# Optimization experiments

Hardware: AMD Instinct MI355X
Metric: run time of the kernel (lower is better)

The kernel has to match this reference:

```python
import jax, jax.numpy as jnp
import numpy as np

DEPTH, E, H, S, V, B = 6, 1024, 16, 2048, 32000, 2
HD = E // H
EPS = 1e-5


def _layernorm(x, w, b):
    mu = jnp.mean(x, axis=-1, keepdims=True)
    var = jnp.mean(jnp.square(x - mu), axis=-1, keepdims=True)
    return (x - mu) * jax.lax.rsqrt(var + EPS) * w + b


def setup_inputs() -> dict:
    key = jax.random.key(0)
    ks = jax.random.split(key, 8)
    std = 0.02
    return {
        "idx": jax.random.randint(ks[0], (B, S), 0, V),
        "tok_emb": jax.random.normal(ks[1], (V, E), jnp.float32) * std,
        "pos_emb": jax.random.normal(ks[2], (S, E), jnp.float32) * std,
        "qkv_w": jax.random.normal(ks[3], (DEPTH, 3 * E, E), jnp.float32) * std,
        "qkv_b": jnp.zeros((DEPTH, 3 * E), jnp.float32),
        "ln1_w": jnp.ones((DEPTH, E), jnp.float32),
        "ln1_b": jnp.zeros((DEPTH, E), jnp.float32),
        "ln2_w": jnp.ones((DEPTH, E), jnp.float32),
        "ln2_b": jnp.zeros((DEPTH, E), jnp.float32),
        "ff1_w": jax.random.normal(ks[4], (DEPTH, 4 * E, E), jnp.float32) * std,
        "ff1_b": jnp.zeros((DEPTH, 4 * E), jnp.float32),
        "ff2_w": jax.random.normal(ks[5], (DEPTH, E, 4 * E), jnp.float32) * std,
        "ff2_b": jnp.zeros((DEPTH, E), jnp.float32),
        "fin_w": jnp.ones((E,), jnp.float32),
        "fin_b": jnp.zeros((E,), jnp.float32),
        "proj_w": jax.random.normal(ks[6], (V, E), jnp.float32) * std,
    }


def _block(x, qkv_w, qkv_b, ln1_w, ln1_b, ln2_w, ln2_b, ff1_w, ff1_b, ff2_w, ff2_b):
    bs, seq, _ = x.shape
    # --- causal MSA (dropout in eval mode -> identity) ---
    xn = _layernorm(x, ln1_w, ln1_b)
    qkv = xn @ qkv_w.T + qkv_b                      # [B,S,3E]
    qkv = qkv.reshape(bs, seq, 3, H, HD)
    q, k, v = (jnp.moveaxis(qkv[:, :, i], 1, 2) for i in range(3))  # [B,H,S,HD]
    scores = jnp.einsum("bhqd,bhkd->bhqk", q, k) / jnp.sqrt(jnp.float32(HD))
    causal = jnp.triu(jnp.ones((seq, seq), bool), k=1)
    scores = jnp.where(causal[None, None], -jnp.inf, scores)
    probs = jax.nn.softmax(scores, axis=-1)
    attn = jnp.einsum("bhqk,bhkd->bqhd", probs, v).reshape(bs, seq, E)
    x = x + attn
    # --- feedforward ---
    xn = _layernorm(x, ln2_w, ln2_b)
    h = jax.nn.gelu(xn @ ff1_w.T + ff1_b, approximate=False)
    x = x + (h @ ff2_w.T + ff2_b)
    return x


def reference(idx, tok_emb, pos_emb, qkv_w, qkv_b, ln1_w, ln1_b, ln2_w, ln2_b,
              ff1_w, ff1_b, ff2_w, ff2_b, fin_w, fin_b, proj_w):
    bs, seq = idx.shape
    x = tok_emb[idx] + pos_emb[jnp.arange(seq)][None]  # [B,S,E]
    for l in range(DEPTH):
        x = _block(x, qkv_w[l], qkv_b[l], ln1_w[l], ln1_b[l], ln2_w[l], ln2_b[l],
                   ff1_w[l], ff1_b[l], ff2_w[l], ff2_b[l])
    x = _layernorm(x, fin_w, fin_b)
    logits = x @ proj_w.T  # [B,S,V], final_proj has no bias
    return logits
```

## Files before the change

kernel.cpp:

```cpp
#include <hip/hip_runtime.h>
#include <hip/hip_bf16.h>

#define DEPTH 6
#define E 1024
#define H 16
#define S 2048
#define V 32000
#define BB 2
#define HD 64
#define NTOK (BB * S)

typedef __attribute__((ext_vector_type(8))) short bf16x8;
typedef __attribute__((ext_vector_type(4))) float f32x4;
typedef unsigned short us;

__device__ inline us f2bf(float f) {
    union { float f; unsigned u; } v; v.f = f;
    unsigned r = v.u + 0x7fff + ((v.u >> 16) & 1);
    return (us)(r >> 16);
}
__device__ inline float bf2f(us b) {
    union { unsigned u; float f; } v; v.u = ((unsigned)b) << 16;
    return v.f;
}

__device__ __forceinline__ void gld16(const us* g, us* l) {
    __builtin_amdgcn_global_load_lds(
        (const __attribute__((address_space(1))) unsigned int*)g,
        (__attribute__((address_space(3))) unsigned int*)l, 16, 0, 0);
}

__global__ __launch_bounds__(256) void cast_kernel(const float* __restrict__ in,
                                                   us* __restrict__ out, int n8) {
    int i = blockIdx.x * 256 + threadIdx.x;
    if (i >= n8) return;
    const float4* p = (const float4*)in + 2 * (size_t)i;
    float4 a = p[0], b = p[1];
    uint4 o;
    o.x = f2bf(a.x) | ((unsigned)f2bf(a.y) << 16);
    o.y = f2bf(a.z) | ((unsigned)f2bf(a.w) << 16);
    o.z = f2bf(b.x) | ((unsigned)f2bf(b.y) << 16);
    o.w = f2bf(b.z) | ((unsigned)f2bf(b.w) << 16);
    ((uint4*)out)[i] = o;
}

__global__ void embed_kernel(const int* __restrict__ idx, const float* __restrict__ tok,
                             const float* __restrict__ pos, float* __restrict__ x) {
    int t = blockIdx.x;
    int s = t & (S - 1);
    int tokid = idx[t];
    int c = threadIdx.x * 4;
    float4 a = *(const float4*)&tok[(size_t)tokid * E + c];
    float4 p = *(const float4*)&pos[(size_t)s * E + c];
    float4 o; o.x = a.x + p.x; o.y = a.y + p.y; o.z = a.z + p.z; o.w = a.w + p.w;
    *(float4*)&x[(size_t)t * E + c] = o;
}

__global__ __launch_bounds__(256) void ln_kernel(const float* __restrict__ x,
                                                 const float* __restrict__ w,
                                                 const float* __restrict__ b,
                                                 us* __restrict__ out) {
    int row = blockIdx.x;
    int tid = threadIdx.x;
    int c = tid * 4;
    float4 v = *(const float4*)&x[(size_t)row * E + c];
    float s  = v.x + v.y + v.z + v.w;
    float sq = v.x * v.x + v.y * v.y + v.z * v.z + v.w * v.w;
    __shared__ float red[8];
    for (int o = 32; o > 0; o >>= 1) { s += __shfl_xor(s, o); sq += __shfl_xor(sq, o); }
    int wave = tid >> 6, lane = tid & 63;
    if (lane == 0) { red[wave] = s; red[4 + wave] = sq; }
    __syncthreads();
    if (tid == 0) {
        red[0] = red[0] + red[1] + red[2] + red[3];
        red[4] = red[4] + red[5] + red[6] + red[7];
    }
    __syncthreads();
    float mean = red[0] * (1.0f / E);
    float var  = red[4] * (1.0f / E) - mean * mean;
    float rstd = rsqrtf(var + 1e-5f);
    float4 wv = *(const float4*)&w[c];
    float4 bv = *(const float4*)&b[c];
    unsigned a0 = f2bf((v.x - mean) * rstd * wv.x + bv.x);
    unsigned a1 = f2bf((v.y - mean) * rstd * wv.y + bv.y);
    unsigned a2 = f2bf((v.z - mean) * rstd * wv.z + bv.z);
    unsigned a3 = f2bf((v.w - mean) * rstd * wv.w + bv.w);
    uint2 o; o.x = a0 | (a1 << 16); o.y = a2 | (a3 << 16);
    *(uint2*)&out[(size_t)row * E + c] = o;
}

#define GPH(dd, fb, STAGE, ISVM, IS12)                                              \
  {                                                                                 \
    bf16x8 afr0[2], afr1[2];                                                        \
    if ((fb) == 0) {                                                                \
      _Pragma("unroll")                                                             \
      for (int n = 0; n < 4; n++)                                                   \
        _Pragma("unroll")                                                           \
        for (int ks = 0; ks < 2; ks++)                                              \
          bfr[n][ks] = *(const bf16x8*)&lds[32768 + (dd) * 16384 +                  \
              (brow + n * 16) * 64 + ((ks * 4 + g4) ^ xg) * 8];                     \
    }                                                                               \
    _Pragma("unroll")                                                               \
    for (int ks = 0; ks < 2; ks++) {                                                \
      afr0[ks] = *(const bf16x8*)&lds[(dd) * 16384 + ((fb) >> 1) * 4096 +           \
          arow0 * 64 + ((ks * 4 + g4) ^ xg) * 8];                                   \
      afr1[ks] = *(const bf16x8*)&lds[(dd) * 16384 + ((fb) >> 1) * 4096 +           \
          arow1 * 64 + ((ks * 4 + g4) ^ xg) * 8];                                   \
    }                                                                               \
    STAGE;                                                                          \
    __builtin_amdgcn_sched_barrier(0);                                              \
    if (IS12) asm volatile("s_waitcnt lgkmcnt(8)" ::: "memory");                    \
    __builtin_amdgcn_s_barrier();                                                   \
    asm volatile("s_waitcnt lgkmcnt(0)" ::: "memory");                              \
    __builtin_amdgcn_sched_barrier(0);                                              \
    __builtin_amdgcn_s_setprio(1);                                                  \
    _Pragma("unroll")                                                               \
    for (int n = 0; n < 4; n++)                                                     \
      _Pragma("unroll")                                                             \
      for (int ks = 0; ks < 2; ks++) {                                              \
        acc[(fb)][n]     = __builtin_amdgcn_mfma_f32_16x16x32_bf16(afr0[ks], bfr[n][ks], acc[(fb)][n], 0, 0, 0);     \
        acc[(fb) + 1][n] = __builtin_amdgcn_mfma_f32_16x16x32_bf16(afr1[ks], bfr[n][ks], acc[(fb) + 1][n], 0, 0, 0); \
      }                                                                             \
    __builtin_amdgcn_s_setprio(0);                                                  \
    __builtin_amdgcn_sched_barrier(0);                                              \
    if (ISVM) asm volatile("s_waitcnt vmcnt(6)" ::: "memory");                      \
    __builtin_amdgcn_s_barrier();                                                   \
  }

template <int OUT_BF16, int ACT_GELU, int HAS_BIAS>
__global__ __launch_bounds__(512, 2) void gemm256(const us* __restrict__ A, int lda,
                                                  const us* __restrict__ Bw, int ldb,
                                                  const float* __restrict__ bias,
                                                  void* __restrict__ outp,
                                                  int M, int N, int K, int ldo) {
    __shared__ us lds[65536];
    int tid = threadIdx.x;
    int nwg = gridDim.x;
    int wgid = blockIdx.x;
    int chunk = nwg >> 3;
    int sw = (wgid & 7) * chunk + (wgid >> 3);
    int MB = M >> 8;
    int bm = (sw % MB) * 256;
    int bn = (sw / MB) * 256;
    int w = tid >> 6, lane = tid & 63;
    int wr = w >> 2, wc = w & 3;
    int l15 = lane & 15, g4 = lane >> 4;
    int xg = l15 & 7;
    int arow0 = (wr ? 32 : 0) + l15;
    int arow1 = arow0 + 16;
    int brow = wc * 64 + l15;
    int NT = K >> 6;

    f32x4 acc[8][4] = {};
    bf16x8 bfr[4][2];

    auto stA = [&](int u, int dd, int h) {
        int uu = (u < NT) ? u : NT - 1;
        #pragma unroll
        for (int i = 0; i < 2; i++) {
            int k = tid + i * 512;
            int q = 2 * h + (k >> 9);
            int r = (k >> 3) & 63;
            int tr = q * 32 + (r & 31) + ((r >> 5) << 7);
            int gp = (k & 7) ^ (r & 7);
            gld16(A + (size_t)(bm + tr) * lda + uu * 64 + gp * 8,
                  &lds[dd * 16384 + h * 8192 + k * 8]);
        }
    };
    auto stB = [&](int u, int dd, int h) {
        int uu = (u < NT) ? u : NT - 1;
        #pragma unroll
        for (int i = 0; i < 2; i++) {
            int k = tid + i * 512;
            int row = h * 128 + (k >> 3);
            int gp = (k & 7) ^ ((k >> 3) & 7);
            gld16(Bw + (size_t)(bn + row) * ldb + uu * 64 + gp * 8,
                  &lds[32768 + dd * 16384 + h * 8192 + k * 8]);
        }
    };

    stB(0, 0, 0); stB(0, 0, 1); stA(0, 0, 0); stA(0, 0, 1);
    stB(1, 1, 0); stB(1, 1, 1); stA(1, 1, 0);
    __builtin_amdgcn_sched_barrier(0);
    asm volatile("s_waitcnt vmcnt(6)" ::: "memory");
    __builtin_amdgcn_s_barrier();

    #pragma unroll 1
    for (int t = 0; t < NT; t += 2) {
        GPH(0, 0, stA(t + 1, 1, 1), 0, 1)
        GPH(0, 2, stB(t + 2, 0, 0), 0, 0)
        GPH(0, 4, stB(t + 2, 0, 1), 0, 0)
        GPH(0, 6, stA(t + 2, 0, 0), 1, 0)
        GPH(1, 0, stA(t + 2, 0, 1), 0, 1)
        GPH(1, 2, stB(t + 3, 1, 0), 0, 0)
        GPH(1, 4, stB(t + 3, 1, 1), 0, 0)
        GPH(1, 6, stA(t + 3, 1, 0), 1, 0)
    }

    float* outf = (float*)outp;
    us* outb = (us*)outp;
    #pragma unroll
    for (int mf = 0; mf < 8; mf++)
        #pragma unroll
        for (int n = 0; n < 4; n++)
            #pragma unroll
            for (int j = 0; j < 4; j++) {
                int r = bm + wr * 128 + mf * 16 + g4 * 4 + j;
                int c = bn + wc * 64 + n * 16 + l15;
                float v = acc[mf][n][j];
                if (HAS_BIAS) v += bias[c];
                if (ACT_GELU) v = 0.5f * v * (1.0f + erff(v * 0.70710678118f));
                if (OUT_BF16) outb[(size_t)r * ldo + c] = f2bf(v);
                else outf[(size_t)r * ldo + c] = v;
            }
}

template <int SPLITK>
__global__ __launch_bounds__(256) void gemm_bf16(const us* __restrict__ A, int lda,
                                                 const us* __restrict__ Bw, int ldb,
                                                 void* __restrict__ outp,
                                                 int M, int N, int K, int ldo) {
    __shared__ us As[2 * 128 * 32];
    __shared__ us Bs[2 * 128 * 32];
    int tid = threadIdx.x;
    int nwg = gridDim.x;
    int chunk = nwg >> 3;
    int wgid = blockIdx.x;
    int sw = (wgid & 7) * chunk + (wgid >> 3);

    int bm, bn;
    us* outb = (us*)outp;
    {
        int kz = sw >> 8;
        int rem = sw & 255;
        bm = (rem & 31) * 128;
        bn = (rem >> 5) * 128;
        A  += (size_t)kz * K;
        Bw += (size_t)kz * K;
        outb += (size_t)kz * M * ldo;
    }

    int wave = tid >> 6, lane = tid & 63;
    int wr = wave >> 1, wc = wave & 1;
    int l15 = lane & 15, g4 = lane >> 4;
    f32x4 acc[4][4] = {};

    for (int k0 = 0; k0 < K; k0 += 64) {
        #pragma unroll
        for (int p4 = 0; p4 < 4; p4++) {
            int p = p4 * 256 + tid;
            int ks = p >> 9, q = p & 511;
            int row = q >> 2, c8 = (q & 3) * 8;
            gld16(&A[(size_t)(bm + row) * lda + k0 + ks * 32 + c8], &As[p * 8]);
            gld16(&Bw[(size_t)(bn + row) * ldb + k0 + ks * 32 + c8], &Bs[p * 8]);
        }
        __syncthreads();
        bf16x8 a[4][2], bfr[4][2];
        #pragma unroll
        for (int m = 0; m < 4; m++)
            #pragma unroll
            for (int ks = 0; ks < 2; ks++)
                a[m][ks] = *(const bf16x8*)&As[ks * 4096 + (wr * 64 + m * 16 + l15) * 32 + g4 * 8];
        #pragma unroll
        for (int n = 0; n < 4; n++)
            #pragma unroll
            for (int ks = 0; ks < 2; ks++)
                bfr[n][ks] = *(const bf16x8*)&Bs[ks * 4096 + (wc * 64 + n * 16 + l15) * 32 + g4 * 8];
        #pragma unroll
        for (int m = 0; m < 4; m++)
            #pragma unroll
            for (int n = 0; n < 4; n++)
                #pragma unroll
                for (int ks = 0; ks < 2; ks++)
                    acc[m][n] = __builtin_amdgcn_mfma_f32_16x16x32_bf16(a[m][ks], bfr[n][ks], acc[m][n], 0, 0, 0);
        __syncthreads();
    }

    #pragma unroll
    for (int m = 0; m < 4; m++)
        #pragma unroll
        for (int n = 0; n < 4; n++)
            #pragma unroll
            for (int j = 0; j < 4; j++) {
                int r = bm + wr * 64 + m * 16 + g4 * 4 + j;
                int c = bn + wc * 64 + n * 16 + l15;
                outb[(size_t)r * ldo + c] = f2bf(acc[m][n][j]);
            }
}

__global__ __launch_bounds__(256) void combine_ff2(const us* __restrict__ p0,
                                                   const us* __restrict__ p1,
                                                   const float* __restrict__ bias,
                                                   float* __restrict__ x) {
    int g = blockIdx.x * 256 + threadIdx.x;
    size_t base = (size_t)g * 8;
    int col = (int)(base & (E - 1));
    uint4 a = *(const uint4*)&p0[base];
    uint4 b = *(const uint4*)&p1[base];
    const us* pa = (const us*)&a;
    const us* pb = (const us*)&b;
    float4 x0 = *(const float4*)&x[base];
    float4 x1 = *(const float4*)&x[base + 4];
    float4 w0 = *(const float4*)&bias[col];
    float4 w1 = *(const float4*)&bias[col + 4];
    x0.x += bf2f(pa[0]) + bf2f(pb[0]) + w0.x;
    x0.y += bf2f(pa[1]) + bf2f(pb[1]) + w0.y;
    x0.z += bf2f(pa[2]) + bf2f(pb[2]) + w0.z;
    x0.w += bf2f(pa[3]) + bf2f(pb[3]) + w0.w;
    x1.x += bf2f(pa[4]) + bf2f(pb[4]) + w1.x;
    x1.y += bf2f(pa[5]) + bf2f(pb[5]) + w1.y;
    x1.z += bf2f(pa[6]) + bf2f(pb[6]) + w1.z;
    x1.w += bf2f(pa[7]) + bf2f(pb[7]) + w1.w;
    *(float4*)&x[base] = x0;
    *(float4*)&x[base + 4] = x1;
}

__global__ __launch_bounds__(256) void transpose_v(const us* __restrict__ qkv,
                                                   us* __restrict__ vT) {
    int kt = blockIdx.x, h = blockIdx.y, b = blockIdx.z;
    int tid = threadIdx.x;
    __shared__ us T[64][72];
    const size_t base = (size_t)b * S * 3072 + 2048 + h * 64;
    int k0 = kt * 64;
    #pragma unroll
    for (int it = 0; it < 2; it++) {
        int p = tid + it * 256;
        int key = p & 63, c8 = (p >> 6) * 8;
        uint4 v = *(const uint4*)&qkv[base + (size_t)(k0 + key) * 3072 + c8];
        us* pv = (us*)&v;
        #pragma unroll
        for (int e = 0; e < 8; e++) T[c8 + e][key] = pv[e];
    }
    __syncthreads();
    const size_t obase = ((size_t)(b * H + h) * 64) * S + k0;
    #pragma unroll
    for (int it = 0; it < 2; it++) {
        int o = tid + it * 256;
        int d = o >> 3, cc = (o & 7) * 8;
        uint4 v = *(const uint4*)&T[d][cc];
        *(uint4*)&vT[obase + (size_t)d * S + cc] = v;
    }
}

__global__ __launch_bounds__(512, 4) void attn_kernel(const us* __restrict__ qkv,
                                                      const us* __restrict__ vT,
                                                      float* __restrict__ x) {
    int qt = blockIdx.x, h = blockIdx.y, b = blockIdx.z;
    int tid = threadIdx.x;
    int w = tid >> 6, lane = tid & 63;
    int l15 = lane & 15, g4 = lane >> 4;
    int s0 = qt * 128;
    int qrow_base = s0 + w * 16;
    const size_t qbase = (size_t)b * S * 3072;
    const size_t vtbase = ((size_t)(b * H + h) * 64) * S;

    __shared__ us K_lds[2][64 * 64];
    __shared__ us VT_lds[2][64 * 64];
    __shared__ us P_lds[8][16 * 72];

    bf16x8 q[2];
    #pragma unroll
    for (int dc = 0; dc < 2; dc++)
        q[dc] = *(const bf16x8*)&qkv[qbase + (size_t)(qrow_base + l15) * 3072 + h * 64 + dc * 32 + 8 * g4];

    f32x4 O[4] = {};
    float m_run[4], l_run[4];
    #pragma unroll
    for (int j = 0; j < 4; j++) { m_run[j] = -INFINITY; l_run[j] = 0.0f; }

    int lastt = 2 * qt + 1;
    {
        int p = tid, row = p >> 3, cc = p & 7;
        int scc = cc ^ (row & 7);
        gld16(&qkv[qbase + (size_t)(0 + row) * 3072 + 1024 + h * 64 + scc * 8], &K_lds[0][p * 8]);
        gld16(&vT[vtbase + (size_t)row * S + 0 + scc * 8], &VT_lds[0][p * 8]);
    }
    __syncthreads();

    for (int t = 0; t <= lastt; t++) {
        int bb = t & 1;
        if (t < lastt) {
            int p = tid, row = p >> 3, cc = p & 7;
            int scc = cc ^ (row & 7);
            gld16(&qkv[qbase + (size_t)((t + 1) * 64 + row) * 3072 + 1024 + h * 64 + scc * 8], &K_lds[bb ^ 1][p * 8]);
            gld16(&vT[vtbase + (size_t)row * S + (t + 1) * 64 + scc * 8], &VT_lds[bb ^ 1][p * 8]);
        }
        int k0 = t * 64;
        if (k0 <= qrow_base + 15) {
            f32x4 sf[4];
            __builtin_amdgcn_s_setprio(1);
            #pragma unroll
            for (int c = 0; c < 4; c++) {
                f32x4 z = {};
                int row = c * 16 + l15;
                #pragma unroll
                for (int dc = 0; dc < 2; dc++) {
                    int ch = (dc * 4 + g4) ^ (row & 7);
                    bf16x8 kb = *(const bf16x8*)&K_lds[bb][row * 64 + ch * 8];
                    z = __builtin_amdgcn_mfma_f32_16x16x32_bf16(q[dc], kb, z, 0, 0, 0);
                }
                sf[c] = z;
            }
            __builtin_amdgcn_s_setprio(0);
            bool needmask = (k0 + 63 > qrow_base);
            float pr[4][4], alpha[4];
            #pragma unroll
            for (int j = 0; j < 4; j++) {
                int qrow = qrow_base + g4 * 4 + j;
                float v0 = sf[0][j] * 0.125f, v1 = sf[1][j] * 0.125f;
                float v2 = sf[2][j] * 0.125f, v3 = sf[3][j] * 0.125f;
                if (needmask) {
                    if (k0 +      l15 > qrow) v0 = -INFINITY;
                    if (k0 + 16 + l15 > qrow) v1 = -INFINITY;
                    if (k0 + 32 + l15 > qrow) v2 = -INFINITY;
                    if (k0 + 48 + l15 > qrow) v3 = -INFINITY;
                }
                float tm = fmaxf(fmaxf(v0, v1), fmaxf(v2, v3));
                tm = fmaxf(tm, __shfl_xor(tm, 1, 16));
                tm = fmaxf(tm, __shfl_xor(tm, 2, 16));
                tm = fmaxf(tm, __shfl_xor(tm, 4, 16));
                tm = fmaxf(tm, __shfl_xor(tm, 8, 16));
                float mnew = fmaxf(m_run[j], tm);
                float p0 = __expf(v0 - mnew), p1 = __expf(v1 - mnew);
                float p2 = __expf(v2 - mnew), p3 = __expf(v3 - mnew);
                float ts = (p0 + p1) + (p2 + p3);
                ts += __shfl_xor(ts, 1, 16);
                ts += __shfl_xor(ts, 2, 16);
                ts += __shfl_xor(ts, 4, 16);
                ts += __shfl_xor(ts, 8, 16);
                alpha[j] = __expf(m_run[j] - mnew);
                l_run[j] = l_run[j] * alpha[j] + ts;
                m_run[j] = mnew;
                pr[0][j] = p0; pr[1][j] = p1; pr[2][j] = p2; pr[3][j] = p3;
            }
            #pragma unroll
            for (int f = 0; f < 4; f++)
                #pragma unroll
                for (int j = 0; j < 4; j++) O[f][j] *= alpha[j];
            us* Pw = &P_lds[w][0];
            #pragma unroll
            for (int c = 0; c < 4; c++)
                #pragma unroll
                for (int j = 0; j < 4; j++)
                    Pw[(g4 * 4 + j) * 72 + c * 16 + l15] = f2bf(pr[c][j]);
            __builtin_amdgcn_s_setprio(1);
            #pragma unroll
            for (int kc = 0; kc < 2; kc++) {
                bf16x8 pa = *(const bf16x8*)&Pw[l15 * 72 + kc * 32 + g4 * 8];
                #pragma unroll
                for (int dt = 0; dt < 4; dt++) {
                    int row = dt * 16 + l15;
                    int ch = (kc * 4 + g4) ^ (row & 7);
                    bf16x8 vb = *(const bf16x8*)&VT_lds[bb][row * 64 + ch * 8];
                    O[dt] = __builtin_amdgcn_mfma_f32_16x16x32_bf16(pa, vb, O[dt], 0, 0, 0);
                }
            }
            __builtin_amdgcn_s_setprio(0);
        }
        __syncthreads();
    }
    #pragma unroll
    for (int dt = 0; dt < 4; dt++)
        #pragma unroll
        for (int j = 0; j < 4; j++) {
            size_t o = ((size_t)b * S + qrow_base + g4 * 4 + j) * E + h * 64 + dt * 16 + l15;
            x[o] += O[dt][j] / l_run[j];
        }
}

extern "C" void kernel_launch(void* const* d_in, const int* in_sizes, int n_in,
                              void* d_out, int out_size, void* d_ws, size_t ws_size,
                              hipStream_t stream) {
    const int*   idx    = (const int*)d_in[0];
    const float* tok    = (const float*)d_in[1];
    const float* pos    = (const float*)d_in[2];
    const float* qkv_w  = (const float*)d_in[3];
    const float* qkv_b  = (const float*)d_in[4];
    const float* ln1_w  = (const float*)d_in[5];
    const float* ln1_b  = (const float*)d_in[6];
    const float* ln2_w  = (const float*)d_in[7];
    const float* ln2_b  = (const float*)d_in[8];
    const float* ff1_w  = (const float*)d_in[9];
    const float* ff1_b  = (const float*)d_in[10];
    const float* ff2_w  = (const float*)d_in[11];
    const float* ff2_b  = (const float*)d_in[12];
    const float* fin_w  = (const float*)d_in[13];
    const float* fin_b  = (const float*)d_in[14];
    const float* proj_w = (const float*)d_in[15];

    char* ws = (char*)d_ws;
    float* x    = (float*)ws;
    us*    xn   = (us*)(ws + 16777216);
    us*    qkvb = (us*)(ws + 25165824);
    us*    hbuf = (us*)(ws + 50331648);
    us*    wbuf = (us*)(ws + 83886080);
    us*    vTb  = (us*)(ws + 92274688);
    us*    pbuf = qkvb;

    embed_kernel<<<NTOK, 256, 0, stream>>>(idx, tok, pos, x);
    for (int l = 0; l < DEPTH; l++) {
        ln_kernel<<<NTOK, 256, 0, stream>>>(x, ln1_w + l * E, ln1_b + l * E, xn);
        cast_kernel<<<1536, 256, 0, stream>>>(qkv_w + (size_t)l * 3 * E * E, wbuf, 3 * E * E / 8);
        gemm256<1, 0, 1><<<192, 512, 0, stream>>>(
            xn, E, wbuf, E, qkv_b + l * 3 * E, qkvb, NTOK, 3 * E, E, 3 * E);
        transpose_v<<<dim3(S / 64, H, BB), 256, 0, stream>>>(qkvb, vTb);
        attn_kernel<<<dim3(S / 128, H, BB), 512, 0, stream>>>(qkvb, vTb, x);
        ln_kernel<<<NTOK, 256, 0, stream>>>(x, ln2_w + l * E, ln2_b + l * E, xn);
        cast_kernel<<<2048, 256, 0, stream>>>(ff1_w + (size_t)l * 4 * E * E, wbuf, 4 * E * E / 8);
        gemm256<1, 1, 1><<<256, 512, 0, stream>>>(
            xn, E, wbuf, E, ff1_b + l * 4 * E, hbuf, NTOK, 4 * E, E, 4 * E);
        cast_kernel<<<2048, 256, 0, stream>>>(ff2_w + (size_t)l * E * 4 * E, wbuf, 4 * E * E / 8);
        gemm_bf16<1><<<512, 256, 0, stream>>>(
            hbuf, 4 * E, wbuf, 4 * E, qkvb, NTOK, E, 2 * E, E);
        combine_ff2<<<2048, 256, 0, stream>>>(qkvb, qkvb + (size_t)NTOK * E, ff2_b + l * E, x);
    }
    ln_kernel<<<NTOK, 256, 0, stream>>>(x, fin_w, fin_b, xn);
    cast_kernel<<<16000, 256, 0, stream>>>(proj_w, pbuf, V * E / 8);
    gemm256<0, 0, 0><<<2000, 512, 0, stream>>>(
        xn, E, pbuf, E, nullptr, d_out, NTOK, V, E, V);
}
```

Baseline: 1.982 ms.

## Use persistent pipelined GEMM for final projection and lazy softmax rescale in attention

Adds a persistent 256-workgroup GEMM for the vocabulary projection that prefetches the next tile's first K-slices while finishing the current tile. This is meant to hide the prologue and epilogue load latency of the 2000-block launch. Separately, the attention kernel skips the running-max update and the O rescale when the new block max stays within 8 of the running max across the wave. That saves exp and multiply work but lets exp values grow up to e^8 before renormalisation.

```diff
diff --git a/kernel.cpp b/kernel.cpp
--- a/kernel.cpp
+++ b/kernel.cpp
@@ -215,6 +215,107 @@
             }
 }
 
+__global__ __launch_bounds__(512, 2) void gemm256p(const us* __restrict__ A, int lda,
+                                                   const us* __restrict__ Bw, int ldb,
+                                                   float* __restrict__ outp,
+                                                   int M, int N, int K, int ldo) {
+    __shared__ us lds[65536];
+    int tid = threadIdx.x;
+    int p = blockIdx.x;
+    int xcd = p & 7, bpx = p >> 3;
+    int MB = M >> 8;
+    int NTILE = MB * (N >> 8);
+    int TPX = NTILE >> 3;
+    int NT = K >> 6;
+
+    int w = tid >> 6, lane = tid & 63;
+    int wr = w >> 2, wc = w & 3;
+    int l15 = lane & 15, g4 = lane >> 4;
+    int xg = l15 & 7;
+    int arow0 = (wr ? 32 : 0) + l15;
+    int arow1 = arow0 + 16;
+    int brow = wc * 64 + l15;
+
+    f32x4 acc[8][4] = {};
+    bf16x8 bfr[4][2];
+
+    auto stA2 = [&](const us* Ab, int u, int dd, int h) {
+        #pragma unroll
+        for (int i = 0; i < 2; i++) {
+            int k = tid + i * 512;
+            int q = 2 * h + (k >> 9);
+            int r = (k >> 3) & 63;
+            int tr = q * 32 + (r & 31) + ((r >> 5) << 7);
+            int gp = (k & 7) ^ (r & 7);
+            gld16(Ab + (size_t)tr * lda + u * 64 + gp * 8,
+                  &lds[dd * 16384 + h * 8192 + k * 8]);
+        }
+    };
+    auto stB2 = [&](const us* Bb, int u, int dd, int h) {
+        #pragma unroll
+        for (int i = 0; i < 2; i++) {
+            int k = tid + i * 512;
+            int row = h * 128 + (k >> 3);
+            int gp = (k & 7) ^ ((k >> 3) & 7);
+            gld16(Bb + (size_t)row * ldb + u * 64 + gp * 8,
+                  &lds[32768 + dd * 16384 + h * 8192 + k * 8]);
+        }
+    };
+
+    int T0 = xcd * TPX + bpx;
+    int bmc = (T0 % MB) * 256, bnc = (T0 / MB) * 256;
+    const us* Ac = A + (size_t)bmc * lda;
+    const us* Bc = Bw + (size_t)bnc * ldb;
+
+    stB2(Bc, 0, 0, 0); stB2(Bc, 0, 0, 1); stA2(Ac, 0, 0, 0); stA2(Ac, 0, 0, 1);
+    stB2(Bc, 1, 1, 0); stB2(Bc, 1, 1, 1); stA2(Ac, 1, 1, 0);
+    __builtin_amdgcn_sched_barrier(0);
+    asm volatile("s_waitcnt vmcnt(6)" ::: "memory");
+    __builtin_amdgcn_s_barrier();
+
+    #pragma unroll 1
+    for (int j = bpx; j < TPX; j += 32) {
+        int jn = j + 32;
+        int Tn = (jn < TPX) ? (xcd * TPX + jn) : (xcd * TPX + j);
+        int bmn = (Tn % MB) * 256, bnn = (Tn / MB) * 256;
+        const us* An = A + (size_t)bmn * lda;
+        const us* Bn = Bw + (size_t)bnn * ldb;
+
+        #pragma unroll 1
+        for (int t = 0; t + 3 < NT; t += 2) {
+            GPH(0, 0, stA2(Ac, t + 1, 1, 1), 0, 1)
+            GPH(0, 2, stB2(Bc, t + 2, 0, 0), 0, 0)
+            GPH(0, 4, stB2(Bc, t + 2, 0, 1), 0, 0)
+            GPH(0, 6, stA2(Ac, t + 2, 0, 0), 1, 0)
+            GPH(1, 0, stA2(Ac, t + 2, 0, 1), 0, 1)
+            GPH(1, 2, stB2(Bc, t + 3, 1, 0), 0, 0)
+            GPH(1, 4, stB2(Bc, t + 3, 1, 1), 0, 0)
+            GPH(1, 6, stA2(Ac, t + 3, 1, 0), 1, 0)
+        }
+        GPH(0, 0, stA2(Ac, NT - 1, 1, 1), 0, 1)
+        GPH(0, 2, stB2(Bn, 0, 0, 0), 0, 0)
+        GPH(0, 4, stB2(Bn, 0, 0, 1), 0, 0)
+        GPH(0, 6, stA2(An, 0, 0, 0), 1, 0)
+        GPH(1, 0, stA2(An, 0, 0, 1), 0, 1)
+        GPH(1, 2, stB2(Bn, 1, 1, 0), 0, 0)
+        GPH(1, 4, stB2(Bn, 1, 1, 1), 0, 0)
+        GPH(1, 6, stA2(An, 1, 1, 0), 1, 0)
+
+        #pragma unroll
+        for (int mf = 0; mf < 8; mf++)
+            #pragma unroll
+            for (int n = 0; n < 4; n++)
+                #pragma unroll
+                for (int jj = 0; jj < 4; jj++) {
+                    int r = bmc + wr * 128 + mf * 16 + g4 * 4 + jj;
+                    int c = bnc + wc * 64 + n * 16 + l15;
+                    outp[(size_t)r * ldo + c] = acc[mf][n][jj];
+                    acc[mf][n][jj] = 0.0f;
+                }
+        Ac = An; Bc = Bn; bmc = bmn; bnc = bnn;
+    }
+}
+
 template <int SPLITK>
 __global__ __launch_bounds__(256) void gemm_bf16(const us* __restrict__ A, int lda,
                                                  const us* __restrict__ Bw, int ldb,
@@ -403,7 +504,7 @@
             }
             __builtin_amdgcn_s_setprio(0);
             bool needmask = (k0 + 63 > qrow_base);
-            float pr[4][4], alpha[4];
+            float tmr[4];
             #pragma unroll
             for (int j = 0; j < 4; j++) {
                 int qrow = qrow_base + g4 * 4 + j;
@@ -420,7 +521,24 @@
                 tm = fmaxf(tm, __shfl_xor(tm, 2, 16));
                 tm = fmaxf(tm, __shfl_xor(tm, 4, 16));
                 tm = fmaxf(tm, __shfl_xor(tm, 8, 16));
-                float mnew = fmaxf(m_run[j], tm);
+                tmr[j] = tm;
+            }
+            bool ok = (tmr[0] <= m_run[0] + 8.0f) && (tmr[1] <= m_run[1] + 8.0f) &&
+                      (tmr[2] <= m_run[2] + 8.0f) && (tmr[3] <= m_run[3] + 8.0f);
+            bool skip = __all(ok);
+            float pr[4][4], alpha[4];
+            #pragma unroll
+            for (int j = 0; j < 4; j++) {
+                int qrow = qrow_base + g4 * 4 + j;
+                float v0 = sf[0][j] * 0.125f, v1 = sf[1][j] * 0.125f;
+                float v2 = sf[2][j] * 0.125f, v3 = sf[3][j] * 0.125f;
+                if (needmask) {
+                    if (k0 +      l15 > qrow) v0 = -INFINITY;
+                    if (k0 + 16 + l15 > qrow) v1 = -INFINITY;
+                    if (k0 + 32 + l15 > qrow) v2 = -INFINITY;
+                    if (k0 + 48 + l15 > qrow) v3 = -INFINITY;
+                }
+                float mnew = skip ? m_run[j] : fmaxf(m_run[j], tmr[j]);
                 float p0 = __expf(v0 - mnew), p1 = __expf(v1 - mnew);
                 float p2 = __expf(v2 - mnew), p3 = __expf(v3 - mnew);
                 float ts = (p0 + p1) + (p2 + p3);
@@ -428,15 +546,21 @@
                 ts += __shfl_xor(ts, 2, 16);
                 ts += __shfl_xor(ts, 4, 16);
                 ts += __shfl_xor(ts, 8, 16);
-                alpha[j] = __expf(m_run[j] - mnew);
-                l_run[j] = l_run[j] * alpha[j] + ts;
-                m_run[j] = mnew;
+                if (skip) {
+                    l_run[j] += ts;
+                } else {
+                    alpha[j] = __expf(m_run[j] - mnew);
+                    l_run[j] = l_run[j] * alpha[j] + ts;
+                    m_run[j] = mnew;
+                }
                 pr[0][j] = p0; pr[1][j] = p1; pr[2][j] = p2; pr[3][j] = p3;
             }
-            #pragma unroll
-            for (int f = 0; f < 4; f++)
+            if (!skip) {
                 #pragma unroll
-                for (int j = 0; j < 4; j++) O[f][j] *= alpha[j];
+                for (int f = 0; f < 4; f++)
+                    #pragma unroll
+                    for (int j = 0; j < 4; j++) O[f][j] *= alpha[j];
+            }
             us* Pw = &P_lds[w][0];
             #pragma unroll
             for (int c = 0; c < 4; c++)
@@ -516,6 +640,6 @@
     }
     ln_kernel<<<NTOK, 256, 0, stream>>>(x, fin_w, fin_b, xn);
     cast_kernel<<<16000, 256, 0, stream>>>(proj_w, pbuf, V * E / 8);
-    gemm256<0, 0, 0><<<2000, 512, 0, stream>>>(
-        xn, E, pbuf, E, nullptr, d_out, NTOK, V, E, V);
-}
+    gemm256p<<<256, 512, 0, stream>>>(
+        xn, E, pbuf, E, (float*)d_out, NTOK, V, E, V);
+}
```

New measurement: 2.054 ms. +3.6%, slower.
